# Performance work log

Hardware: AMD Instinct MI355X
Metric: run time of the kernel (lower is better)

Reference implementation:

```python
import jax, jax.numpy as jnp
import numpy as np

NEG = -1e9
EPS = 1e-5


def _layernorm(x, g, b):
    m = x.mean(-1, keepdims=True)
    v = ((x - m) ** 2).mean(-1, keepdims=True)
    return (x - m) / jnp.sqrt(v + EPS) * g + b


def _layer(h_aug, H_inc, mask_neg, W1, W1_hat, ctx1, W2, W2_hat, W3, g, b):
    # h_aug: (T, H), H_inc/mask_neg: (T, E)
    H = h_aug.shape[-1]
    scale = 1.0 / jnp.sqrt(jnp.asarray(H, h_aug.dtype))
    # Stage 1: node -> hyperedge attention
    proj_hat = h_aug @ W1_hat.T                       # (T, H)
    raw = (proj_hat * ctx1).sum(-1) * scale           # (T,)
    score = raw[:, None] + mask_neg                   # (T, E)
    alpha = jax.nn.softmax(score, axis=0) * H_inc     # (T, E)
    hyper = alpha.T @ (h_aug @ W1.T)                  # (E, H)
    # Stage 2: hyperedge -> node attention
    proj2_hat = hyper @ W2_hat.T                      # (E, H)
    score_ne = (h_aug @ W3.T) @ proj2_hat.T * scale + mask_neg  # (T, E)
    beta = jax.nn.softmax(score_ne, axis=1) * H_inc   # (T, E)
    out = beta @ (hyper @ W2.T)                       # (T, H)
    return _layernorm(out + h_aug, g, b)


def reference(node_emb, H_inc, membership, W1, W1_hat, ctx1, W2, W2_hat, W3, ln_g, ln_b, region_init):
    B, N, H = node_emb.shape
    R = region_init.shape[0]
    L = W1.shape[0]
    mask_neg = jnp.where(H_inc == 0, NEG, 0.0).astype(node_emb.dtype)
    counts = jax.ops.segment_sum(jnp.ones((N,), node_emb.dtype), membership, num_segments=R)
    safe_counts = jnp.maximum(counts, 1.0)

    def per_sample(h):  # h: (N, H)
        sums = jax.ops.segment_sum(h, membership, num_segments=R)     # (R, H)
        reg = jnp.where(counts[:, None] > 0, sums / safe_counts[:, None], 0.0)
        reg = reg + region_init
        h_aug = jnp.concatenate([h, reg], axis=0)                     # (N+R, H)
        for l in range(L):
            h_aug = _layer(h_aug, H_inc, mask_neg, W1[l], W1_hat[l], ctx1[l],
                           W2[l], W2_hat[l], W3[l], ln_g[l], ln_b[l])
        return h_aug[:N]

    return jax.vmap(per_sample)(node_emb)


def setup_inputs() -> dict:
    key = jax.random.key(0)
    ks = jax.random.split(key, 12)
    B, N, R, E, H, L = 4, 8000, 16, 1024, 128, 2
    T = N + R
    w_std = 1.0 / np.sqrt(H)
    node_emb = jax.random.normal(ks[0], (B, N, H), dtype=jnp.float32)
    H_inc = (jax.random.uniform(ks[1], (T, E)) < 0.05).astype(jnp.float32)
    membership = jax.random.randint(ks[2], (N,), 0, R, dtype=jnp.int32)
    W1 = jax.random.normal(ks[3], (L, H, H), dtype=jnp.float32) * w_std
    W1_hat = jax.random.normal(ks[4], (L, H, H), dtype=jnp.float32) * w_std
    ctx1 = jax.random.normal(ks[5], (L, H), dtype=jnp.float32) * 0.02
    W2 = jax.random.normal(ks[6], (L, H, H), dtype=jnp.float32) * w_std
    W2_hat = jax.random.normal(ks[7], (L, H, H), dtype=jnp.float32) * w_std
    W3 = jax.random.normal(ks[8], (L, H, H), dtype=jnp.float32) * w_std
    ln_g = jnp.ones((L, H), dtype=jnp.float32)
    ln_b = jnp.zeros((L, H), dtype=jnp.float32)
    region_init = jax.random.normal(ks[9], (R, H), dtype=jnp.float32) * 0.02
    return {"node_emb": node_emb, "H_inc": H_inc, "membership": membership,
            "W1": W1, "W1_hat": W1_hat, "ctx1": ctx1, "W2": W2, "W2_hat": W2_hat,
            "W3": W3, "ln_g": ln_g, "ln_b": ln_b, "region_init": region_init}
```

## Files before the change

kernel.cpp:

```cpp
#include <hip/hip_runtime.h>

#define HD 128
#define CAPE 768
#define MAXR 16
#define NB_RS 128
#define RF_CH 16
#define KSTR 136
#define VSTR 72

typedef unsigned short u16;
typedef unsigned long long u64;
typedef __attribute__((ext_vector_type(8))) short bf16x8;
typedef __attribute__((ext_vector_type(4))) float f32x4;
typedef __attribute__((ext_vector_type(4))) unsigned u32x4;

__device__ inline float b2f(unsigned u){ return __uint_as_float(u << 16); }
__device__ inline u16 f2b(float x){
  unsigned u = __float_as_uint(x);
  return (u16)((u + 0x7fffu + ((u >> 16) & 1u)) >> 16);
}

__device__ inline float waveSum(float v){ for(int o=32;o;o>>=1) v += __shfl_down(v,o); return v; }
__device__ inline float waveMax(float v){ for(int o=32;o;o>>=1) v = fmaxf(v,__shfl_down(v,o)); return v; }

__device__ inline float blockSum128(float v, float* red){
  int j = threadIdx.x;
  float s = waveSum(v);
  __syncthreads();
  if ((j & 63) == 0) red[j >> 6] = s;
  __syncthreads();
  return red[0] + red[1];
}
__device__ inline float blockMax128(float v, float* red){
  int j = threadIdx.x;
  float s = waveMax(v);
  __syncthreads();
  if ((j & 63) == 0) red[j >> 6] = s;
  __syncthreads();
  return fmaxf(red[0], red[1]);
}

__global__ void k_count(const int* __restrict__ memb, int N, int* __restrict__ counts){
  __shared__ int h[64];
  int tid = threadIdx.x;
  if (tid < 64) h[tid] = 0;
  __syncthreads();
  for (int t = blockIdx.x*blockDim.x + tid; t < N; t += gridDim.x*blockDim.x)
    atomicAdd(&h[memb[t]], 1);
  __syncthreads();
  if (tid < 64){ int v = h[tid]; if (v) atomicAdd(&counts[tid], v); }
}

__global__ __launch_bounds__(128) void k_regsum_fast(const float* __restrict__ node,
                        const int* __restrict__ memb, int N, int R,
                        float* __restrict__ partials){
  int b = blockIdx.y, j = threadIdx.x, blk = blockIdx.x;
  int nb = gridDim.x;
  int per = (N + nb - 1) / nb;
  int t0 = blk * per;
  int t1 = t0 + per; if (t1 > N) t1 = N;
  float acc[MAXR];
  #pragma unroll
  for (int i = 0; i < MAXR; ++i) acc[i] = 0.f;
  const float* base = node + (long)b*N*HD + j;
  #pragma unroll 4
  for (int t = t0; t < t1; ++t){
    float v = base[(long)t*HD];
    int r = memb[t];
    #pragma unroll
    for (int i = 0; i < MAXR; ++i) acc[i] += (i == r) ? v : 0.f;
  }
  float* dst = partials + ((long)(b*nb + blk)*R)*HD + j;
  #pragma unroll
  for (int i = 0; i < MAXR; ++i)
    if (i < R) dst[(long)i*HD] = acc[i];
}

__global__ void k_regsum_lds(const float* __restrict__ node, const int* __restrict__ memb,
                             int N, int R, float* __restrict__ partials, int nb){
  extern __shared__ float acc[];
  int b = blockIdx.y, j = threadIdx.x;
  for (int r = 0; r < R; ++r) acc[r*HD + j] = 0.f;
  int per = (N + gridDim.x - 1) / gridDim.x;
  int t0 = blockIdx.x * per;
  int t1 = t0 + per; if (t1 > N) t1 = N;
  for (int t = t0; t < t1; ++t){
    int r = memb[t];
    acc[r*HD + j] += node[((long)b*N + t)*HD + j];
  }
  for (int r = 0; r < R; ++r)
    atomicAdd(&partials[((long)(b*nb)*R + r)*HD + j], acc[r*HD + j]);
}

__global__ __launch_bounds__(128) void k_regfin1(const float* __restrict__ partials,
                         int nb, int redN, int total, float* __restrict__ red2){
  int c = blockIdx.y;
  int i = blockIdx.x*128 + threadIdx.x;
  if (i >= total) return;
  int R_HD = total / ((int)gridDim.x * 0 + 1); (void)R_HD;
  int j = i % HD;
  int br = i / HD;
  int RHD = 0; (void)RHD;
  int per = (redN + RF_CH - 1) / RF_CH;
  int k0 = c*per, k1 = k0 + per; if (k1 > redN) k1 = redN;
  (void)j; (void)br; (void)k0; (void)k1; (void)nb; (void)red2;
}

__global__ __launch_bounds__(128) void k_regfin1b(const float* __restrict__ partials,
                         int nb, int redN, int R, int total, float* __restrict__ red2){
  int c = blockIdx.y;
  int i = blockIdx.x*128 + threadIdx.x;
  if (i >= total) return;
  int j = i % HD;
  int r = (i / HD) % R;
  int b = i / (HD * R);
  int per = (redN + RF_CH - 1) / RF_CH;
  int k0 = c*per, k1 = k0 + per; if (k1 > redN) k1 = redN;
  float s = 0.f;
  for (int blk = k0; blk < k1; ++blk)
    s += partials[((long)(b*nb + blk)*R + r)*HD + j];
  red2[(long)c*total + i] = s;
}

__global__ void k_regfin2(const float* __restrict__ red2, int total,
                          const int* __restrict__ counts,
                          const float* __restrict__ rinit, float* __restrict__ h_aug,
                          int N, int R, int T, int B){
  int i = blockIdx.x*blockDim.x + threadIdx.x;
  if (i >= total) return;
  int j = i % HD; int r = (i/HD) % R; int b = i/(HD*R);
  float s = 0.f;
  #pragma unroll
  for (int c = 0; c < RF_CH; ++c)
    s += red2[(long)c*total + i];
  int cnt = counts[r];
  float v = (cnt > 0) ? s / (float)cnt : 0.f;
  v += rinit[r*HD + j];
  h_aug[((long)b*T + N + r)*HD + j] = v;
}

__global__ __launch_bounds__(128) void k_copyraw(const float* __restrict__ node,
                      const float* __restrict__ v, float* __restrict__ h_aug,
                      float* __restrict__ raw, int N, int T, float scale){
  int t = blockIdx.x, b = blockIdx.y, j = threadIdx.x;
  __shared__ float red[2];
  long rowb = (long)b*T + t;
  float x;
  if (t < N){ x = node[((long)b*N + t)*HD + j]; h_aug[rowb*HD + j] = x; }
  else      { x = h_aug[rowb*HD + j]; }
  float s = blockSum128(x * v[j], red);
  if (j == 0) raw[rowb] = s * scale;
}

__global__ __launch_bounds__(256) void k_maskbuild(const float* __restrict__ Hinc, int E, int MW,
                        u64* __restrict__ maskw){
  int t = blockIdx.x;
  int wv = threadIdx.x >> 6, lane = threadIdx.x & 63;
  const float* hrow = Hinc + (long)t*E;
  for (int w = wv; w < MW; w += 4){
    int e = w*64 + lane;
    bool f = (e < E) && (hrow[e] != 0.f);
    u64 mk = __ballot(f);
    if (lane == 0) maskw[(long)t*MW + w] = mk;
  }
}

__global__ __launch_bounds__(256) void k_colbuild2(const u64* __restrict__ maskw, int T, int MW,
                           u16* __restrict__ colidx, int* __restrict__ colcnt){
  int e = blockIdx.x;
  int w = e >> 6, bit = e & 63;
  int j = threadIdx.x;
  int lane = j & 63, wv = j >> 6;
  __shared__ int wsum[4];
  int c = 0;
  for (int base = 0; base < T; base += 256){
    int t = base + j;
    bool f = (t < T) && ((maskw[(long)t*MW + w] >> bit) & 1ull);
    u64 mk = __ballot(f);
    if (lane == 0) wsum[wv] = __popcll(mk);
    __syncthreads();
    int pre = 0;
    #pragma unroll
    for (int k = 0; k < 4; ++k) pre += (k < wv) ? wsum[k] : 0;
    int tot = wsum[0] + wsum[1] + wsum[2] + wsum[3];
    if (f){
      int pos = c + pre + (int)__popcll(mk & ((1ull << lane) - 1ull));
      if (pos < CAPE) colidx[(long)e*CAPE + pos] = (u16)t;
    }
    c += tot;
    __syncthreads();
  }
  if (j == 0) colcnt[e] = (c < CAPE) ? c : CAPE;
}

__global__ void k_ctxv(const float* __restrict__ ctx1, const float* __restrict__ W1h,
                       float* __restrict__ v){
  int l = blockIdx.x, k = threadIdx.x;
  float a = 0.f;
  for (int j = 0; j < HD; ++j) a += ctx1[l*HD + j] * W1h[((long)l*HD + j)*HD + k];
  v[l*HD + k] = a;
}

__global__ void k_mm128(const float* __restrict__ W2h, const float* __restrict__ W3,
                        float* __restrict__ MqT){
  int n = blockIdx.x, l = blockIdx.y, k = threadIdx.x;
  const float* A = W2h + (long)l*HD*HD;
  const float* Bm = W3 + (long)l*HD*HD;
  float s = 0.f;
  for (int j = 0; j < HD; ++j) s += A[(long)j*HD + n] * Bm[(long)j*HD + k];
  MqT[((long)l*HD + n)*HD + k] = s;
}

__global__ __launch_bounds__(256) void k_gemmM(const float* __restrict__ A,
                       const float* __restrict__ Wa, const float* __restrict__ Wb,
                       u16* __restrict__ Ca, u16* __restrict__ Cb, int M){
  const float* W = blockIdx.y ? Wb : Wa;
  u16* C = blockIdx.y ? Cb : Ca;
  __shared__ __align__(16) u16 Ws[128][KSTR];
  __shared__ __align__(16) u16 As[64][KSTR];
  int tid = threadIdx.x;
  int row0 = blockIdx.x * 64;
  for (int i = tid; i < 128*128; i += 256){
    int r = i >> 7, c = i & 127;
    Ws[r][c] = f2b(W[(long)r*HD + c]);
  }
  for (int i = tid; i < 64*128; i += 256){
    int r = i >> 7, c = i & 127;
    int gr = row0 + r;
    As[r][c] = (gr < M) ? f2b(A[(long)gr*HD + c]) : (u16)0;
  }
  __syncthreads();

  int wave = tid >> 6, lane = tid & 63;
  int wr0 = wave * 16;
  int frow = lane & 15;
  int koff = (lane >> 4) * 8;
  f32x4 acc[8];
  #pragma unroll
  for (int f = 0; f < 8; ++f) acc[f] = (f32x4){0.f,0.f,0.f,0.f};

  #pragma unroll
  for (int ks = 0; ks < 4; ++ks){
    int kc = ks*32 + koff;
    bf16x8 av = *(const bf16x8*)&As[wr0 + frow][kc];
    #pragma unroll
    for (int f = 0; f < 8; ++f){
      bf16x8 bv = *(const bf16x8*)&Ws[f*16 + frow][kc];
      acc[f] = __builtin_amdgcn_mfma_f32_16x16x32_bf16(av, bv, acc[f], 0, 0, 0);
    }
  }

  int orow = wr0 + (lane >> 4) * 4;
  #pragma unroll
  for (int f = 0; f < 8; ++f){
    int col = f*16 + frow;
    #pragma unroll
    for (int i = 0; i < 4; ++i){
      int gr = row0 + orow + i;
      if (gr < M) C[(long)gr*HD + col] = f2b(acc[f][i]);
    }
  }
}

__global__ __launch_bounds__(256) void k_gemmW2T(const float* __restrict__ W2,
                       const u16* __restrict__ hyb, u16* __restrict__ hw2t, int E){
  int b = blockIdx.y;
  int e0 = blockIdx.x * 64;
  __shared__ __align__(16) u16 As[128][KSTR];
  __shared__ __align__(16) u16 Bs[64][KSTR];
  int tid = threadIdx.x;
  for (int i = tid; i < 128*128; i += 256){
    int r = i >> 7, c = i & 127;
    As[r][c] = f2b(W2[(long)r*HD + c]);
  }
  {
    int er = tid >> 2, q = (tid & 3)*32;
    if (e0 + er < E){
      const uint4* src = (const uint4*)(hyb + ((long)b*E + e0 + er)*HD + q);
      uint4 w0 = src[0], w1 = src[1], w2 = src[2], w3 = src[3];
      *(uint4*)&Bs[er][q]    = w0;
      *(uint4*)&Bs[er][q+8]  = w1;
      *(uint4*)&Bs[er][q+16] = w2;
      *(uint4*)&Bs[er][q+24] = w3;
    } else {
      uint4 z = {0,0,0,0};
      *(uint4*)&Bs[er][q] = z; *(uint4*)&Bs[er][q+8] = z;
      *(uint4*)&Bs[er][q+16] = z; *(uint4*)&Bs[er][q+24] = z;
    }
  }
  __syncthreads();
  int wv = tid >> 6, lane = tid & 63;
  int lc = lane & 15, lg = lane >> 4;
  f32x4 acc[2][4];
  #pragma unroll
  for (int mt=0;mt<2;++mt)
    #pragma unroll
    for (int nf=0;nf<4;++nf) acc[mt][nf] = (f32x4){0.f,0.f,0.f,0.f};
  #pragma unroll
  for (int mt=0;mt<2;++mt){
    int hr = wv*32 + mt*16 + lc;
    #pragma unroll
    for (int ks=0;ks<4;++ks){
      bf16x8 av = *(const bf16x8*)&As[hr][ks*32 + lg*8];
      #pragma unroll
      for (int nf=0;nf<4;++nf){
        bf16x8 bv = *(const bf16x8*)&Bs[nf*16+lc][ks*32 + lg*8];
        acc[mt][nf] = __builtin_amdgcn_mfma_f32_16x16x32_bf16(av, bv, acc[mt][nf], 0,0,0);
      }
    }
  }
  #pragma unroll
  for (int mt=0;mt<2;++mt){
    #pragma unroll
    for (int nf=0;nf<4;++nf){
      #pragma unroll
      for (int i=0;i<4;++i){
        int h = wv*32 + mt*16 + lg*4 + i;
        int e = e0 + nf*16 + lc;
        if (e < E) hw2t[((long)b*HD + h)*E + e] = f2b(acc[mt][nf][i]);
      }
    }
  }
}

__global__ __launch_bounds__(128) void k_edge(int swz, const float* __restrict__ raw,
                      const u16* __restrict__ proj1b,
                      const int* __restrict__ colcnt, const u16* __restrict__ colidx,
                      u16* __restrict__ hyb, int T, int E){
  int bi = blockIdx.x;
  int b, e;
  if (swz){ int x = bi & 7; b = x >> 1; e = ((bi >> 3) << 1) | (x & 1); }
  else    { b = bi / E; e = bi - b*E; }
  int j = threadIdx.x;
  __shared__ float red[2];
  __shared__ float wls[CAPE];
  __shared__ int   tls[CAPE];
  int c = colcnt[e]; if (c > CAPE) c = CAPE;
  const u16* ci = colidx + (long)e*CAPE;
  const float* rawb = raw + (long)b*T;
  long orow = ((long)b*E + e)*HD + j;
  if (c <= 0){ hyb[orow] = 0; return; }
  float lm = -1e30f;
  for (int i = j; i < c; i += 128){
    int t = ci[i];
    float v = rawb[t];
    tls[i] = t;
    wls[i] = v;
    lm = fmaxf(lm, v);
  }
  float m = blockMax128(lm, red);
  float lz = 0.f;
  for (int i = j; i < c; i += 128){
    float w = __expf(wls[i] - m);
    wls[i] = w;
    lz += w;
  }
  float Z = blockSum128(lz, red);
  float invZ = 1.f / Z;
  const u16* pb = proj1b + (long)b*T*HD + j;
  float a0=0.f,a1=0.f,a2=0.f,a3=0.f;
  int i = 0;
  for (; i + 4 <= c; i += 4){
    a0 += wls[i]   * b2f(pb[(long)tls[i]  *HD]);
    a1 += wls[i+1] * b2f(pb[(long)tls[i+1]*HD]);
    a2 += wls[i+2] * b2f(pb[(long)tls[i+2]*HD]);
    a3 += wls[i+3] * b2f(pb[(long)tls[i+3]*HD]);
  }
  for (; i < c; ++i) a0 += wls[i] * b2f(pb[(long)tls[i]*HD]);
  hyb[orow] = f2b(((a0+a1)+(a2+a3)) * invZ);
}

__global__ __launch_bounds__(256) void k_flashp(
      const u16* __restrict__ qtb, const u16* __restrict__ hyb, const u16* __restrict__ hw2t,
      const u64* __restrict__ maskw,
      u16* __restrict__ Opart, float* __restrict__ mpart, float* __restrict__ lpart,
      int T, int E, int half, float scale){
  int b = blockIdx.y, Bc = gridDim.y;
  int s = blockIdx.z, nsplit = gridDim.z;
  int t0 = blockIdx.x * 64;
  int tid = threadIdx.x;
  int wv = tid >> 6, lane = tid & 63;
  int lc = lane & 15, lg = lane >> 4;

  __shared__ __align__(16) u16 Ks[64][KSTR];
  __shared__ __align__(16) u16 Vs[128][VSTR];

  int MW = (E + 63) >> 6;
  int ntile = (E + 63) / 64;
  int et0 = s * half;
  int etend = (s == nsplit-1) ? ntile : ((s+1)*half < ntile ? (s+1)*half : ntile);

  int qrow = t0 + wv*16 + lc;
  bf16x8 qf[4];
  if (qrow < T){
    const u16* qr = qtb + ((long)b*T + qrow)*HD + lg*8;
    #pragma unroll
    for (int ks = 0; ks < 4; ++ks) qf[ks] = *(const bf16x8*)(qr + ks*32);
  } else {
    #pragma unroll
    for (int ks = 0; ks < 4; ++ks) qf[ks] = (bf16x8){0,0,0,0,0,0,0,0};
  }

  float m_s = -1e30f, l_s = 0.f;
  f32x4 Oa[8];
  #pragma unroll
  for (int f=0;f<8;++f) Oa[f] = (f32x4){0.f,0.f,0.f,0.f};

  const u16* hyB = hyb + (long)b*E*HD;
  const u16* vtB = hw2t + (long)b*HD*E;

  int kr = tid >> 2, kq = (tid & 3)*32;
  int vh = tid >> 1, vo = (tid & 1)*32;

  uint4 kreg0, kreg1, kreg2, kreg3, vreg0, vreg1, vreg2, vreg3;
  const uint4 zz = make_uint4(0u,0u,0u,0u);

  if (et0 < etend){
    int e0 = et0*64;
    if (e0 + kr < E){
      const uint4* sp = (const uint4*)(hyB + (long)(e0+kr)*HD + kq);
      kreg0=sp[0]; kreg1=sp[1]; kreg2=sp[2]; kreg3=sp[3];
    } else { kreg0=zz; kreg1=zz; kreg2=zz; kreg3=zz; }
    if (e0 + vo + 31 < E){
      const uint4* sp = (const uint4*)(vtB + (long)vh*E + e0 + vo);
      vreg0=sp[0]; vreg1=sp[1]; vreg2=sp[2]; vreg3=sp[3];
    } else {
      union { uint4 v[4]; u16 s[32]; } u;
      #pragma unroll
      for (int k=0;k<32;++k){ int e=e0+vo+k; u.s[k] = (e<E)? vtB[(long)vh*E+e] : (u16)0; }
      vreg0=u.v[0]; vreg1=u.v[1]; vreg2=u.v[2]; vreg3=u.v[3];
    }
  }

  for (int et = et0; et < etend; ++et){
    *(uint4*)&Ks[kr][kq]    = kreg0;
    *(uint4*)&Ks[kr][kq+8]  = kreg1;
    *(uint4*)&Ks[kr][kq+16] = kreg2;
    *(uint4*)&Ks[kr][kq+24] = kreg3;
    {
      int eb0 = vo;        int ne0 = eb0>>4; int ka0 = (ne0>>1)*32 + ((eb0>>2)&3)*8 + (ne0&1)*4;
      int eb1 = vo + 8;    int ne1 = eb1>>4; int ka1 = (ne1>>1)*32 + ((eb1>>2)&3)*8 + (ne1&1)*4;
      int eb2 = vo + 16;   int ne2 = eb2>>4; int ka2 = (ne2>>1)*32 + ((eb2>>2)&3)*8 + (ne2&1)*4;
      int eb3 = vo + 24;   int ne3 = eb3>>4; int ka3 = (ne3>>1)*32 + ((eb3>>2)&3)*8 + (ne3&1)*4;
      *(uint2*)&Vs[vh][ka0]   = make_uint2(vreg0.x, vreg0.y);
      *(uint2*)&Vs[vh][ka0+8] = make_uint2(vreg0.z, vreg0.w);
      *(uint2*)&Vs[vh][ka1]   = make_uint2(vreg1.x, vreg1.y);
      *(uint2*)&Vs[vh][ka1+8] = make_uint2(vreg1.z, vreg1.w);
      *(uint2*)&Vs[vh][ka2]   = make_uint2(vreg2.x, vreg2.y);
      *(uint2*)&Vs[vh][ka2+8] = make_uint2(vreg2.z, vreg2.w);
      *(uint2*)&Vs[vh][ka3]   = make_uint2(vreg3.x, vreg3.y);
      *(uint2*)&Vs[vh][ka3+8] = make_uint2(vreg3.z, vreg3.w);
    }
    __syncthreads();
    if (et + 1 < etend){
      int e0 = (et+1)*64;
      if (e0 + kr < E){
        const uint4* sp = (const uint4*)(hyB + (long)(e0+kr)*HD + kq);
        kreg0=sp[0]; kreg1=sp[1]; kreg2=sp[2]; kreg3=sp[3];
      } else { kreg0=zz; kreg1=zz; kreg2=zz; kreg3=zz; }
      if (e0 + vo + 31 < E){
        const uint4* sp = (const uint4*)(vtB + (long)vh*E + e0 + vo);
        vreg0=sp[0]; vreg1=sp[1]; vreg2=sp[2]; vreg3=sp[3];
      } else {
        union { uint4 v[4]; u16 s[32]; } u;
        #pragma unroll
        for (int k=0;k<32;++k){ int e=e0+vo+k; u.s[k] = (e<E)? vtB[(long)vh*E+e] : (u16)0; }
        vreg0=u.v[0]; vreg1=u.v[1]; vreg2=u.v[2]; vreg3=u.v[3];
      }
    }

    u64 mw = (qrow < T) ? maskw[(long)qrow*MW + et] : 0ull;

    f32x4 accS[4];
    #pragma unroll
    for (int ne=0;ne<4;++ne) accS[ne] = (f32x4){0.f,0.f,0.f,0.f};
    __builtin_amdgcn_s_setprio(1);
    #pragma unroll
    for (int ks=0;ks<4;++ks){
      #pragma unroll
      for (int ne=0;ne<4;++ne){
        bf16x8 kv = *(const bf16x8*)&Ks[ne*16+lc][ks*32 + lg*8];
        accS[ne] = __builtin_amdgcn_mfma_f32_16x16x32_bf16(kv, qf[ks], accS[ne], 0,0,0);
      }
    }
    __builtin_amdgcn_s_setprio(0);

    unsigned lo = (unsigned)mw, hi = (unsigned)(mw >> 32);
    unsigned nib[4];
    nib[0] = (lo >> (lg*4)) & 0xFu;
    nib[1] = (lo >> (16 + lg*4)) & 0xFu;
    nib[2] = (hi >> (lg*4)) & 0xFu;
    nib[3] = (hi >> (16 + lg*4)) & 0xFu;

    float p[4][4];
    float mx = -3e30f;
    #pragma unroll
    for (int ne=0;ne<4;++ne){
      #pragma unroll
      for (int r=0;r<4;++r){
        float sv = ((nib[ne] >> r) & 1u) ? accS[ne][r]*scale : -3e30f;
        p[ne][r] = sv;
        mx = fmaxf(mx, sv);
      }
    }
    mx = fmaxf(mx, __shfl_xor(mx, 16));
    mx = fmaxf(mx, __shfl_xor(mx, 32));

    float corr = 1.f;
    if (!__all(mx <= m_s + 8.f)){
      float mn = fmaxf(m_s, mx);
      corr = __expf(m_s - mn);
      m_s = mn;
      float corrO[4];
      #pragma unroll
      for (int i=0;i<4;++i) corrO[i] = __shfl(corr, lg*4 + i, 16);
      #pragma unroll
      for (int f=0;f<8;++f){
        #pragma unroll
        for (int i=0;i<4;++i) Oa[f][i] *= corrO[i];
      }
    }

    float ls = 0.f;
    #pragma unroll
    for (int ne=0;ne<4;++ne){
      #pragma unroll
      for (int r=0;r<4;++r){
        float pv = __expf(p[ne][r] - m_s);
        p[ne][r] = pv;
        ls += pv;
      }
    }
    ls += __shfl_xor(ls, 16);
    ls += __shfl_xor(ls, 32);
    l_s = l_s*corr + ls;

    unsigned pk00, pk01, pk10, pk11, pk20, pk21, pk30, pk31;
    asm("v_cvt_pk_bf16_f32 %0, %1, %2" : "=v"(pk00) : "v"(p[0][0]), "v"(p[0][1]));
    asm("v_cvt_pk_bf16_f32 %0, %1, %2" : "=v"(pk01) : "v"(p[0][2]), "v"(p[0][3]));
    asm("v_cvt_pk_bf16_f32 %0, %1, %2" : "=v"(pk10) : "v"(p[1][0]), "v"(p[1][1]));
    asm("v_cvt_pk_bf16_f32 %0, %1, %2" : "=v"(pk11) : "v"(p[1][2]), "v"(p[1][3]));
    asm("v_cvt_pk_bf16_f32 %0, %1, %2" : "=v"(pk20) : "v"(p[2][0]), "v"(p[2][1]));
    asm("v_cvt_pk_bf16_f32 %0, %1, %2" : "=v"(pk21) : "v"(p[2][2]), "v"(p[2][3]));
    asm("v_cvt_pk_bf16_f32 %0, %1, %2" : "=v"(pk30) : "v"(p[3][0]), "v"(p[3][1]));
    asm("v_cvt_pk_bf16_f32 %0, %1, %2" : "=v"(pk31) : "v"(p[3][2]), "v"(p[3][3]));

    __builtin_amdgcn_s_setprio(1);
    {
      u32x4 w0v = { pk00, pk01, pk10, pk11 };
      bf16x8 pa0 = __builtin_bit_cast(bf16x8, w0v);
      #pragma unroll
      for (int f=0;f<8;++f){
        bf16x8 vb = *(const bf16x8*)&Vs[f*16+lc][lg*8];
        Oa[f] = __builtin_amdgcn_mfma_f32_16x16x32_bf16(pa0, vb, Oa[f], 0,0,0);
      }
      u32x4 w1v = { pk20, pk21, pk30, pk31 };
      bf16x8 pa1 = __builtin_bit_cast(bf16x8, w1v);
      #pragma unroll
      for (int f=0;f<8;++f){
        bf16x8 vb = *(const bf16x8*)&Vs[f*16+lc][32 + lg*8];
        Oa[f] = __builtin_amdgcn_mfma_f32_16x16x32_bf16(pa1, vb, Oa[f], 0,0,0);
      }
    }
    __builtin_amdgcn_s_setprio(0);
    __syncthreads();
  }

  u16* Ob = Opart + (((long)s*Bc + b)*T)*HD;
  #pragma unroll
  for (int i=0;i<4;++i){
    int t = t0 + wv*16 + lg*4 + i;
    if (t >= T) continue;
    #pragma unroll
    for (int f=0;f<8;++f)
      Ob[(long)t*HD + f*16 + lc] = f2b(Oa[f][i]);
  }
  if (lg == 0 && qrow < T){
    long mlrow = ((long)s*Bc + b)*T + qrow;
    mpart[mlrow] = m_s;
    lpart[mlrow] = l_s;
  }
}

__global__ __launch_bounds__(128) void k_merge(
      const u16* __restrict__ Opart, const float* __restrict__ mpart, const float* __restrict__ lpart,
      int nsplit,
      const float* __restrict__ lng, const float* __restrict__ lnb,
      const float* __restrict__ vnext, float* __restrict__ rawnext, int writeRaw,
      float* __restrict__ h_aug, float* __restrict__ out,
      int T, int N, int writeOut, float scale){
  int t = blockIdx.x, b = blockIdx.y, j = threadIdx.x;
  int Bc = gridDim.y;
  __shared__ float red[2];
  long r0 = ((long)b)*T + t;
  long r1 = ((long)Bc + b)*T + t;
  float m0 = mpart[r0], l0 = lpart[r0];
  float m1 = (nsplit > 1) ? mpart[r1] : -1e30f;
  float l1 = (nsplit > 1) ? lpart[r1] : 0.f;
  float M = fmaxf(m0, m1);
  float c0 = __expf(m0 - M), c1 = __expf(m1 - M);
  float l = l0*c0 + l1*c1;
  float inv = (l > 0.f) ? 1.f/l : 0.f;
  float o = b2f(Opart[r0*HD + j]) * c0;
  if (nsplit > 1) o += b2f(Opart[r1*HD + j]) * c1;
  o *= inv;
  long rowb = (long)b*T + t;
  float x = o + h_aug[rowb*HD + j];
  float mean = blockSum128(x, red) * (1.f/HD);
  float d = x - mean;
  float var = blockSum128(d*d, red) * (1.f/HD);
  float y = d * rsqrtf(var + 1e-5f) * lng[j] + lnb[j];
  if (writeOut){
    if (t < N) out[((long)b*N + t)*HD + j] = y;
  } else {
    h_aug[rowb*HD + j] = y;
  }
  if (writeRaw){
    float s = blockSum128(y * vnext[j], red);
    if (j == 0) rawnext[rowb] = s * scale;
  }
}

extern "C" void kernel_launch(void* const* d_in, const int* in_sizes, int n_in,
                              void* d_out, int out_size, void* d_ws, size_t ws_size,
                              hipStream_t stream) {
  const float* node_emb = (const float*)d_in[0];
  const float* Hinc     = (const float*)d_in[1];
  const int*   memb     = (const int*)d_in[2];
  const float* W1       = (const float*)d_in[3];
  const float* W1h      = (const float*)d_in[4];
  const float* ctx1     = (const float*)d_in[5];
  const float* W2       = (const float*)d_in[6];
  const float* W2h      = (const float*)d_in[7];
  const float* W3       = (const float*)d_in[8];
  const float* lng      = (const float*)d_in[9];
  const float* lnb      = (const float*)d_in[10];
  const float* rinit    = (const float*)d_in[11];
  float* out = (float*)d_out;

  const int N  = in_sizes[2];
  const int Hd = in_sizes[3] / in_sizes[5];
  const int L  = in_sizes[5] / Hd;
  const int R  = in_sizes[11] / Hd;
  const int B  = in_sizes[0] / (N * Hd);
  const int T  = N + R;
  const int E  = in_sizes[1] / T;
  const int MW = (E + 63) / 64;
  const float scale = 1.0f / sqrtf((float)Hd);

  char* p = (char*)d_ws;
  auto carve = [&](size_t bytes){ char* r = p; p += (bytes + 255) & ~(size_t)255; return (void*)r; };
  float* h_aug  = (float*)carve((size_t)B*T*Hd*4);
  u16*   proj1b = (u16*)  carve((size_t)B*T*Hd*2);
  u16*   qtb    = (u16*)  carve((size_t)B*T*Hd*2);
  u16*   hyb    = (u16*)  carve((size_t)B*E*Hd*2);
  u16*   hw2t   = (u16*)  carve((size_t)B*Hd*E*2);
  float* MqT    = (float*)carve((size_t)L*Hd*Hd*4);
  float* rawb   = (float*)carve((size_t)B*T*4);
  float* vbuf   = (float*)carve((size_t)L*Hd*4);
  u64*   maskw  = (u64*)  carve((size_t)T*MW*8);
  int* counts   = (int*)carve((size_t)R*4);
  int* col_cnt  = (int*)carve((size_t)E*4);
  u16* col_idx  = (u16*)carve((size_t)E*CAPE*2);
  float* mpart  = (float*)carve((size_t)2*B*T*4);
  float* lpart  = (float*)carve((size_t)2*B*T*4);
  float* red2   = (float*)carve((size_t)RF_CH*B*MAXR*Hd*4);

  size_t used = (size_t)(p - (char*)d_ws);
  size_t rem  = (ws_size > used) ? (ws_size - used) : 0;
  size_t needP  = (size_t)B*NB_RS*R*Hd*4;
  size_t needO2 = (size_t)2*B*T*Hd*2;
  size_t need2 = needP > needO2 ? needP : needO2;
  int SPLIT = (rem >= need2) ? 2 : 1;
  float* partials = (float*)p;
  u16*   Opart    = (u16*)p;

  hipMemsetAsync(counts, 0, (size_t)R*4, stream);

  k_count<<<32, 256, 0, stream>>>(memb, N, counts);

  int total = B*R*Hd;
  int redN;
  if (R <= MAXR){
    k_regsum_fast<<<dim3(NB_RS, B), 128, 0, stream>>>(node_emb, memb, N, R, partials);
    redN = NB_RS;
  } else {
    hipMemsetAsync(partials, 0, (size_t)B*R*Hd*4, stream);
    k_regsum_lds<<<dim3(16, B), Hd, (size_t)R*Hd*4, stream>>>(node_emb, memb, N, R, partials, NB_RS);
    redN = 1;
  }
  k_regfin1b<<<dim3((total+127)/128, RF_CH), 128, 0, stream>>>(partials, NB_RS, redN, R, total, red2);
  k_regfin2<<<(total+255)/256, 256, 0, stream>>>(red2, total, counts, rinit, h_aug, N, R, T, B);

  k_maskbuild<<<T, 256, 0, stream>>>(Hinc, E, MW, maskw);
  k_colbuild2<<<E, 256, 0, stream>>>(maskw, T, MW, col_idx, col_cnt);

  k_ctxv<<<L, Hd, 0, stream>>>(ctx1, W1h, vbuf);
  k_mm128<<<dim3(Hd, L), Hd, 0, stream>>>(W2h, W3, MqT);
  k_copyraw<<<dim3(T, B), 128, 0, stream>>>(node_emb, vbuf, h_aug, rawb, N, T, scale);

  int MT = B*T;
  int gTm = (MT + 63)/64;
  int gTf = (T + 63)/64;
  int gEt = (E + 63)/64;
  int ntile = (E + 63)/64;
  int half = (ntile + SPLIT - 1)/SPLIT;
  int swzE = (B == 4 && (E & 1) == 0) ? 1 : 0;
  for (int l = 0; l < L; ++l){
    size_t wo = (size_t)l*Hd*Hd;
    k_gemmM<<<dim3(gTm, 2), 256, 0, stream>>>(h_aug, W1 + wo, MqT + wo, proj1b, qtb, MT);
    k_edge<<<B*E, 128, 0, stream>>>(swzE, rawb, proj1b, col_cnt, col_idx, hyb, T, E);
    k_gemmW2T<<<dim3(gEt, B), 256, 0, stream>>>(W2 + wo, hyb, hw2t, E);
    k_flashp<<<dim3(gTf, B, SPLIT), 256, 0, stream>>>(qtb, hyb, hw2t, maskw,
                                    Opart, mpart, lpart, T, E, half, scale);
    int writeRaw = (l < L-1) ? 1 : 0;
    const float* vnext = vbuf + (size_t)((l+1 < L) ? (l+1) : l)*Hd;
    k_merge<<<dim3(T, B), 128, 0, stream>>>(Opart, mpart, lpart, SPLIT,
                                    lng + wo/Hd, lnb + wo/Hd,
                                    vnext, rawb, writeRaw,
                                    h_aug, out, T, N, (l == L-1) ? 1 : 0, scale);
  }
}
```

Baseline: 396.6 us.

## Restructure edge aggregation to one wave per batch sharing column indices

Replaces the per-(batch,edge) 128-thread edge kernel with a 256-thread block per edge in which each of four waves handles one batch sample. The column index list is loaded once into shared memory and shared across the batch. Softmax reductions become wave-level shuffles with no block barriers, and each lane gathers two bf16 values per 32-bit load. The intent is to cut block count, synchronisation and gather instructions, at the cost of more shared memory per block and half-width lanes per gather row. It also deletes an unused dead kernel.

After: 452.5 us. +14.1%, slower.

```diff
diff --git a/kernel.cpp b/kernel.cpp
--- a/kernel.cpp
+++ b/kernel.cpp
@@ -15,6 +15,7 @@
 typedef __attribute__((ext_vector_type(4))) unsigned u32x4;
 
 __device__ inline float b2f(unsigned u){ return __uint_as_float(u << 16); }
+__device__ inline float b2fhi(unsigned u){ return __uint_as_float(u & 0xffff0000u); }
 __device__ inline u16 f2b(float x){
   unsigned u = __float_as_uint(x);
   return (u16)((u + 0x7fffu + ((u >> 16) & 1u)) >> 16);
@@ -22,6 +23,8 @@
 
 __device__ inline float waveSum(float v){ for(int o=32;o;o>>=1) v += __shfl_down(v,o); return v; }
 __device__ inline float waveMax(float v){ for(int o=32;o;o>>=1) v = fmaxf(v,__shfl_down(v,o)); return v; }
+__device__ inline float waveAllMax(float v){ for(int o=32;o;o>>=1) v = fmaxf(v,__shfl_xor(v,o)); return v; }
+__device__ inline float waveAllSum(float v){ for(int o=32;o;o>>=1) v += __shfl_xor(v,o); return v; }
 
 __device__ inline float blockSum128(float v, float* red){
   int j = threadIdx.x;
@@ -90,20 +93,6 @@
   }
   for (int r = 0; r < R; ++r)
     atomicAdd(&partials[((long)(b*nb)*R + r)*HD + j], acc[r*HD + j]);
-}
-
-__global__ __launch_bounds__(128) void k_regfin1(const float* __restrict__ partials,
-                         int nb, int redN, int total, float* __restrict__ red2){
-  int c = blockIdx.y;
-  int i = blockIdx.x*128 + threadIdx.x;
-  if (i >= total) return;
-  int R_HD = total / ((int)gridDim.x * 0 + 1); (void)R_HD;
-  int j = i % HD;
-  int br = i / HD;
-  int RHD = 0; (void)RHD;
-  int per = (redN + RF_CH - 1) / RF_CH;
-  int k0 = c*per, k1 = k0 + per; if (k1 > redN) k1 = redN;
-  (void)j; (void)br; (void)k0; (void)k1; (void)nb; (void)red2;
 }
 
 __global__ __launch_bounds__(128) void k_regfin1b(const float* __restrict__ partials,
@@ -323,51 +312,59 @@
   }
 }
 
-__global__ __launch_bounds__(128) void k_edge(int swz, const float* __restrict__ raw,
+__global__ __launch_bounds__(256) void k_edge4(const float* __restrict__ raw,
                       const u16* __restrict__ proj1b,
                       const int* __restrict__ colcnt, const u16* __restrict__ colidx,
-                      u16* __restrict__ hyb, int T, int E){
-  int bi = blockIdx.x;
-  int b, e;
-  if (swz){ int x = bi & 7; b = x >> 1; e = ((bi >> 3) << 1) | (x & 1); }
-  else    { b = bi / E; e = bi - b*E; }
-  int j = threadIdx.x;
-  __shared__ float red[2];
-  __shared__ float wls[CAPE];
+                      u16* __restrict__ hyb, int T, int E, int B){
+  int e = blockIdx.x;
+  int b = blockIdx.y*4 + (threadIdx.x >> 6);
+  int lane = threadIdx.x & 63;
+  int w = threadIdx.x >> 6;
   __shared__ int   tls[CAPE];
+  __shared__ float wls[4][CAPE];
   int c = colcnt[e]; if (c > CAPE) c = CAPE;
   const u16* ci = colidx + (long)e*CAPE;
+  for (int i = threadIdx.x; i < c; i += 256) tls[i] = ci[i];
+  __syncthreads();
+  if (b >= B) return;
+  unsigned* orow = (unsigned*)(hyb + ((long)b*E + e)*HD) + lane;
+  if (c <= 0){ orow[0] = 0u; orow[64] = 0u; return; }
   const float* rawb = raw + (long)b*T;
-  long orow = ((long)b*E + e)*HD + j;
-  if (c <= 0){ hyb[orow] = 0; return; }
   float lm = -1e30f;
-  for (int i = j; i < c; i += 128){
-    int t = ci[i];
-    float v = rawb[t];
-    tls[i] = t;
-    wls[i] = v;
+  for (int i = lane; i < c; i += 64){
+    float v = rawb[tls[i]];
+    wls[w][i] = v;
     lm = fmaxf(lm, v);
   }
-  float m = blockMax128(lm, red);
+  float m = waveAllMax(lm);
   float lz = 0.f;
-  for (int i = j; i < c; i += 128){
-    float w = __expf(wls[i] - m);
-    wls[i] = w;
-    lz += w;
-  }
-  float Z = blockSum128(lz, red);
+  for (int i = lane; i < c; i += 64){
+    float x = __expf(wls[w][i] - m);
+    wls[w][i] = x;
+    lz += x;
+  }
+  float Z = waveAllSum(lz);
   float invZ = 1.f / Z;
-  const u16* pb = proj1b + (long)b*T*HD + j;
-  float a0=0.f,a1=0.f,a2=0.f,a3=0.f;
+  const u16* pb = proj1b + (long)b*T*HD + 2*lane;
+  float a00=0.f,a01=0.f,a10=0.f,a11=0.f;
   int i = 0;
-  for (; i + 4 <= c; i += 4){
-    a0 += wls[i]   * b2f(pb[(long)tls[i]  *HD]);
-    a1 += wls[i+1] * b2f(pb[(long)tls[i+1]*HD]);
-    a2 += wls[i+2] * b2f(pb[(long)tls[i+2]*HD]);
-    a3 += wls[i+3] * b2f(pb[(long)tls[i+3]*HD]);
-  }
-  for (; i < c; ++i) a0 += wls[i] * b2f(pb[(long)tls[i]*HD]);
-  hyb[orow] = f2b(((a0+a1)+(a2+a3)) * invZ);
+  for (; i + 2 <= c; i += 2){
+    int t0v = tls[i], t1v = tls[i+1];
+    float w0 = wls[w][i], w1 = wls[w][i+1];
+    unsigned u0 = *(const unsigned*)(pb + (long)t0v*HD);
+    unsigned u1 = *(const unsigned*)(pb + (long)t1v*HD);
+    a00 += w0 * b2f(u0 & 0xffffu);  a01 += w0 * b2fhi(u0);
+    a10 += w1 * b2f(u1 & 0xffffu);  a11 += w1 * b2fhi(u1);
+  }
+  if (i < c){
+    float w0 = wls[w][i];
+    unsigned u0 = *(const unsigned*)(pb + (long)tls[i]*HD);
+    a00 += w0 * b2f(u0 & 0xffffu);  a01 += w0 * b2fhi(u0);
+  }
+  float o0 = (a00 + a10) * invZ;
+  float o1 = (a01 + a11) * invZ;
+  orow[0] = (unsigned)f2b(o0) | ((unsigned)f2b(o1) << 16);
+  (void)0;
 }
 
 __global__ __launch_bounds__(256) void k_flashp(
@@ -705,11 +702,10 @@
   int gEt = (E + 63)/64;
   int ntile = (E + 63)/64;
   int half = (ntile + SPLIT - 1)/SPLIT;
-  int swzE = (B == 4 && (E & 1) == 0) ? 1 : 0;
   for (int l = 0; l < L; ++l){
     size_t wo = (size_t)l*Hd*Hd;
     k_gemmM<<<dim3(gTm, 2), 256, 0, stream>>>(h_aug, W1 + wo, MqT + wo, proj1b, qtb, MT);
-    k_edge<<<B*E, 128, 0, stream>>>(swzE, rawb, proj1b, col_cnt, col_idx, hyb, T, E);
+    k_edge4<<<dim3(E, (B+3)/4), 256, 0, stream>>>(rawb, proj1b, col_cnt, col_idx, hyb, T, E, B);
     k_gemmW2T<<<dim3(gEt, B), 256, 0, stream>>>(W2 + wo, hyb, hw2t, E);
     k_flashp<<<dim3(gTf, B, SPLIT), 256, 0, stream>>>(qtb, hyb, hw2t, maskw,
                                     Opart, mpart, lpart, T, E, half, scale);
```
